# Kernel tuning notes

Measured on AMD Instinct MI355X. Metric: run time of the kernel, lower is better.

Reference implementation:

```python
import jax, jax.numpy as jnp
import numpy as np

LEVEL = 256
BLOCKS = 8
THRESH = 10.0


def setup_inputs() -> dict:
    key = jax.random.key(0)
    img = jax.random.randint(key, (16, 1024, 1024), 0, LEVEL).astype(jnp.float32)
    return {"img": img}


def _clahe(img):
    B, H, W = img.shape
    bm, bn = H // BLOCKS, W // BLOCKS
    v = img.astype(jnp.int32)  # pixel values 0..255, used as histogram bins

    # ---- per-block histograms via one flat scatter-add (segment_sum) ----
    bi = jnp.arange(H) // bm                      # block row per pixel row
    bj = jnp.arange(W) // bn                      # block col per pixel col
    blk = bi[:, None] * BLOCKS + bj[None, :]      # [H, W] block id
    seg = (jnp.arange(B)[:, None, None] * (BLOCKS * BLOCKS) + blk[None]) * LEVEL + v
    hists = jax.ops.segment_sum(
        jnp.ones((B * H * W,), jnp.float32), seg.reshape(-1),
        num_segments=B * BLOCKS * BLOCKS * LEVEL)
    hists = hists.reshape(B, BLOCKS, BLOCKS, LEVEL)

    # ---- clip histogram: redistribute excess above threshold uniformly ----
    # threshold_value = sum(hists)/LEVEL*threshold ; block sum is bm*bn exactly
    tv = (bm * bn) / LEVEL * THRESH
    total_extra = jnp.sum(jnp.maximum(hists - tv, 0.0), axis=-1, keepdims=True)
    mean_extra = total_extra / LEVEL
    # int() truncation of non-negative values == floor
    clip = jnp.floor(jnp.where(hists >= tv, tv + mean_extra, hists + mean_extra))

    # ---- CDF -> uint8 mapping table per block ----
    cdf = jnp.cumsum(clip, axis=-1) * ((LEVEL - 1) / (bm * bn))
    maps = (jnp.floor(cdf).astype(jnp.int32) % 256).astype(jnp.float32)  # [B,BLOCKS,BLOCKS,LEVEL]

    # ---- per-pixel bilinear blend of 2x2 neighboring block maps ----
    ii = jnp.arange(H, dtype=jnp.float32)
    jj = jnp.arange(W, dtype=jnp.float32)
    # Python int() truncates toward zero, so r,c are always >= 0
    r = jnp.trunc((ii - bm / 2) / bm).astype(jnp.int32)   # [H]
    c = jnp.trunc((jj - bn / 2) / bn).astype(jnp.int32)   # [W]
    x1 = (ii - (r.astype(jnp.float32) + 0.5) * bm) / bm   # [H]
    y1 = (jj - (c.astype(jnp.float32) + 0.5) * bn) / bn   # [W]
    rp = jnp.minimum(r + 1, BLOCKS - 1)
    cp = jnp.minimum(c + 1, BLOCKS - 1)
    # on last block row/col the original falls back to 1-D / nearest interp:
    x1e = jnp.where(r >= BLOCKS - 1, 0.0, x1)[:, None]    # [H,1]
    y1e = jnp.where(c >= BLOCKS - 1, 0.0, y1)[None, :]    # [1,W]

    bidx = jnp.arange(B)[:, None, None]

    def gather(rr, cc):  # maps[b, rr[i], cc[j], v[b,i,j]] -> [B,H,W]
        return maps[bidx, rr[None, :, None], cc[None, None, :], v]

    lu = gather(r, c)
    lb = gather(rp, c)
    ru = gather(r, cp)
    rb = gather(rp, cp)
    out = (1 - y1e) * ((1 - x1e) * lu + x1e * lb) + y1e * ((1 - x1e) * ru + x1e * rb)
    # final .astype('uint8') cast
    return (jnp.trunc(out).astype(jnp.int32) % 256).astype(jnp.float32)


def reference(img) -> jnp.ndarray:
    return _clahe(img)
```

## Files before the change

### kernel.cpp

```cpp
#include <hip/hip_runtime.h>
#include <hip/hip_bf16.h>

#define LEVEL 256
#define BLOCKS 8

__global__ __launch_bounds__(256) void clahe_hist_kernel(const float* __restrict__ img,
                                                         float* __restrict__ maps) {
    __shared__ int   hist[256];
    __shared__ float red[256];
    __shared__ float scan[256];
    __shared__ float s_me;

    const int t   = threadIdx.x;
    const int bid = blockIdx.x;
    const int b   = bid >> 6;
    const int blk = bid & 63;
    const int br  = blk >> 3;
    const int bc  = blk & 7;

    hist[t] = 0;
    __syncthreads();

    const size_t base = (size_t)b * 1048576 + (size_t)(br * 128) * 1024 + (size_t)(bc * 128);
    const float* p = img + base;
    for (int it = 0; it < 16; ++it) {
        int idx = it * 256 + t;
        int y   = idx >> 5;
        int x   = (idx & 31) * 4;
        float4 v = *(const float4*)(p + (size_t)y * 1024 + x);
        atomicAdd(&hist[(int)v.x], 1);
        atomicAdd(&hist[(int)v.y], 1);
        atomicAdd(&hist[(int)v.z], 1);
        atomicAdd(&hist[(int)v.w], 1);
    }
    __syncthreads();

    const float tv = 640.0f;
    float h = (float)hist[t];
    float extra = fmaxf(h - tv, 0.0f);
    red[t] = extra;
    __syncthreads();
    for (int off = 128; off > 0; off >>= 1) {
        if (t < off) red[t] += red[t + off];
        __syncthreads();
    }
    if (t == 0) s_me = red[0] * (1.0f / 256.0f);
    __syncthreads();
    const float me = s_me;
    float clip = floorf(((h >= tv) ? tv : h) + me);

    scan[t] = clip;
    __syncthreads();
    for (int off = 1; off < 256; off <<= 1) {
        float add = (t >= off) ? scan[t - off] : 0.0f;
        __syncthreads();
        scan[t] += add;
        __syncthreads();
    }
    float cdf = scan[t] * (255.0f / 16384.0f);
    int m = ((int)floorf(cdf)) & 255;
    maps[(size_t)bid * 256 + t] = (float)m;
}

__global__ __launch_bounds__(256) void clahe_map_kernel(const float* __restrict__ img,
                                                        const float* __restrict__ maps,
                                                        float* __restrict__ out) {
#pragma clang fp contract(off)
    __shared__ float m_lu[256], m_lb[256], m_ru[256], m_rb[256];

    const int t  = threadIdx.x;
    const int b  = blockIdx.z;
    const int i0 = blockIdx.y * 64;
    const int j0 = blockIdx.x * 64;

    const int r  = (i0 >= 64) ? ((i0 - 64) >> 7) : 0;
    const int c  = (j0 >= 64) ? ((j0 - 64) >> 7) : 0;
    const int rp = min(r + 1, BLOCKS - 1);
    const int cp = min(c + 1, BLOCKS - 1);
    const bool rEdge = (r >= BLOCKS - 1);
    const bool cEdge = (c >= BLOCKS - 1);

    const float* mb = maps + (size_t)b * 64 * 256;
    m_lu[t] = mb[(r  * 8 + c ) * 256 + t];
    m_lb[t] = mb[(rp * 8 + c ) * 256 + t];
    m_ru[t] = mb[(r  * 8 + cp) * 256 + t];
    m_rb[t] = mb[(rp * 8 + cp) * 256 + t];
    __syncthreads();

    const size_t ibase = (size_t)b * 1048576;
    const int row_in = t >> 4;
    const int col4   = (t & 15) * 4;

    for (int it = 0; it < 4; ++it) {
        const int i = i0 + it * 16 + row_in;
        const int j = j0 + col4;
        const float4 px = *(const float4*)(img + ibase + (size_t)i * 1024 + j);

        float x1 = rEdge ? 0.0f : ((float)i - (float)(r * 128 + 64)) * 0.0078125f;

        float vals[4] = {px.x, px.y, px.z, px.w};
        float4 o4;
        float* ov = (float*)&o4;
        for (int k = 0; k < 4; ++k) {
            const int jj = j + k;
            float y1 = cEdge ? 0.0f : ((float)jj - (float)(c * 128 + 64)) * 0.0078125f;
            const int vv = (int)vals[k];
            const float lu = m_lu[vv];
            const float lb = m_lb[vv];
            const float ru = m_ru[vv];
            const float rb = m_rb[vv];
            float o = (1.0f - y1) * ((1.0f - x1) * lu + x1 * lb)
                    + y1 * ((1.0f - x1) * ru + x1 * rb);
            ov[k] = (float)(((int)o) & 255);
        }
        *(float4*)(out + ibase + (size_t)i * 1024 + j) = o4;
    }
}

extern "C" void kernel_launch(void* const* d_in, const int* in_sizes, int n_in,
                              void* d_out, int out_size, void* d_ws, size_t ws_size,
                              hipStream_t stream) {
    const float* img = (const float*)d_in[0];
    float* out = (float*)d_out;
    float* maps = (float*)d_ws;

    clahe_hist_kernel<<<dim3(1024), dim3(256), 0, stream>>>(img, maps);
    clahe_map_kernel<<<dim3(16, 16, 16), dim3(256), 0, stream>>>(img, maps, out);
}
```

Baseline: 125.4 us.

## Cache uint8 copy of image in hist pass and pack four maps into float4 LDS

While building histograms, the first kernel also writes a uint8 copy of the image into workspace. The map kernel then reads that compact copy instead of the float image, cutting its input traffic to a quarter. It also interleaves the four neighbouring block maps into one float4 shared-memory table, so each pixel needs a single LDS load. The cost is an extra 16 MB written in the hist kernel, and the fast path runs only if the workspace is large enough.

```diff
diff --git a/kernel.cpp b/kernel.cpp
--- a/kernel.cpp
+++ b/kernel.cpp
@@ -5,7 +5,8 @@
 #define BLOCKS 8
 
 __global__ __launch_bounds__(256) void clahe_hist_kernel(const float* __restrict__ img,
-                                                         float* __restrict__ maps) {
+                                                         float* __restrict__ maps,
+                                                         unsigned char* __restrict__ u8img) {
     __shared__ int   hist[256];
     __shared__ float red[256];
     __shared__ float scan[256];
@@ -23,15 +24,23 @@
 
     const size_t base = (size_t)b * 1048576 + (size_t)(br * 128) * 1024 + (size_t)(bc * 128);
     const float* p = img + base;
+    unsigned char* q8 = u8img ? (u8img + base) : nullptr;
     for (int it = 0; it < 16; ++it) {
         int idx = it * 256 + t;
         int y   = idx >> 5;
         int x   = (idx & 31) * 4;
         float4 v = *(const float4*)(p + (size_t)y * 1024 + x);
-        atomicAdd(&hist[(int)v.x], 1);
-        atomicAdd(&hist[(int)v.y], 1);
-        atomicAdd(&hist[(int)v.z], 1);
-        atomicAdd(&hist[(int)v.w], 1);
+        int va = (int)v.x, vb = (int)v.y, vc = (int)v.z, vd = (int)v.w;
+        atomicAdd(&hist[va], 1);
+        atomicAdd(&hist[vb], 1);
+        atomicAdd(&hist[vc], 1);
+        atomicAdd(&hist[vd], 1);
+        if (q8) {
+            uchar4 pk;
+            pk.x = (unsigned char)va; pk.y = (unsigned char)vb;
+            pk.z = (unsigned char)vc; pk.w = (unsigned char)vd;
+            *(uchar4*)(q8 + (size_t)y * 1024 + x) = pk;
+        }
     }
     __syncthreads();
 
@@ -62,11 +71,13 @@
     maps[(size_t)bid * 256 + t] = (float)m;
 }
 
-__global__ __launch_bounds__(256) void clahe_map_kernel(const float* __restrict__ img,
+template <bool U8>
+__global__ __launch_bounds__(256) void clahe_map_kernel(const float* __restrict__ imgf,
+                                                        const unsigned char* __restrict__ img8,
                                                         const float* __restrict__ maps,
                                                         float* __restrict__ out) {
 #pragma clang fp contract(off)
-    __shared__ float m_lu[256], m_lb[256], m_ru[256], m_rb[256];
+    __shared__ float4 m4[256];
 
     const int t  = threadIdx.x;
     const int b  = blockIdx.z;
@@ -81,10 +92,13 @@
     const bool cEdge = (c >= BLOCKS - 1);
 
     const float* mb = maps + (size_t)b * 64 * 256;
-    m_lu[t] = mb[(r  * 8 + c ) * 256 + t];
-    m_lb[t] = mb[(rp * 8 + c ) * 256 + t];
-    m_ru[t] = mb[(r  * 8 + cp) * 256 + t];
-    m_rb[t] = mb[(rp * 8 + cp) * 256 + t];
+    {
+        float lu = mb[(r  * 8 + c ) * 256 + t];
+        float lb = mb[(rp * 8 + c ) * 256 + t];
+        float ru = mb[(r  * 8 + cp) * 256 + t];
+        float rb = mb[(rp * 8 + cp) * 256 + t];
+        m4[t] = make_float4(lu, lb, ru, rb);
+    }
     __syncthreads();
 
     const size_t ibase = (size_t)b * 1048576;
@@ -94,23 +108,27 @@
     for (int it = 0; it < 4; ++it) {
         const int i = i0 + it * 16 + row_in;
         const int j = j0 + col4;
-        const float4 px = *(const float4*)(img + ibase + (size_t)i * 1024 + j);
 
-        float x1 = rEdge ? 0.0f : ((float)i - (float)(r * 128 + 64)) * 0.0078125f;
+        int vv[4];
+        if (U8) {
+            uchar4 px = *(const uchar4*)(img8 + ibase + (size_t)i * 1024 + j);
+            vv[0] = px.x; vv[1] = px.y; vv[2] = px.z; vv[3] = px.w;
+        } else {
+            float4 px = *(const float4*)(imgf + ibase + (size_t)i * 1024 + j);
+            vv[0] = (int)px.x; vv[1] = (int)px.y; vv[2] = (int)px.z; vv[3] = (int)px.w;
+        }
 
-        float vals[4] = {px.x, px.y, px.z, px.w};
+        const float x1  = rEdge ? 0.0f : ((float)i - (float)(r * 128 + 64)) * 0.0078125f;
+        const float x0  = 1.0f - x1;
+
         float4 o4;
         float* ov = (float*)&o4;
         for (int k = 0; k < 4; ++k) {
             const int jj = j + k;
-            float y1 = cEdge ? 0.0f : ((float)jj - (float)(c * 128 + 64)) * 0.0078125f;
-            const int vv = (int)vals[k];
-            const float lu = m_lu[vv];
-            const float lb = m_lb[vv];
-            const float ru = m_ru[vv];
-            const float rb = m_rb[vv];
-            float o = (1.0f - y1) * ((1.0f - x1) * lu + x1 * lb)
-                    + y1 * ((1.0f - x1) * ru + x1 * rb);
+            const float y1 = cEdge ? 0.0f : ((float)jj - (float)(c * 128 + 64)) * 0.0078125f;
+            const float4 q = m4[vv[k]];
+            float o = (1.0f - y1) * (x0 * q.x + x1 * q.y)
+                    + y1 * (x0 * q.z + x1 * q.w);
             ov[k] = (float)(((int)o) & 255);
         }
         *(float4*)(out + ibase + (size_t)i * 1024 + j) = o4;
@@ -124,6 +142,17 @@
     float* out = (float*)d_out;
     float* maps = (float*)d_ws;
 
-    clahe_hist_kernel<<<dim3(1024), dim3(256), 0, stream>>>(img, maps);
-    clahe_map_kernel<<<dim3(16, 16, 16), dim3(256), 0, stream>>>(img, maps, out);
+    const size_t maps_bytes = (size_t)1024 * 256 * sizeof(float);
+    const size_t u8_bytes   = (size_t)16 * 1024 * 1024;
+    const bool use_u8 = ws_size >= maps_bytes + u8_bytes;
+    unsigned char* u8img = use_u8 ? ((unsigned char*)d_ws + maps_bytes) : nullptr;
+
+    clahe_hist_kernel<<<dim3(1024), dim3(256), 0, stream>>>(img, maps, u8img);
+    if (use_u8) {
+        clahe_map_kernel<true><<<dim3(16, 16, 16), dim3(256), 0, stream>>>(
+            nullptr, u8img, maps, out);
+    } else {
+        clahe_map_kernel<false><<<dim3(16, 16, 16), dim3(256), 0, stream>>>(
+            img, nullptr, maps, out);
+    }
 }
```

Result: no change. 124.0 us (-1.1%).

## Stage image as uint8 in workspace, per-wave histograms, packed LUT table

Applied to the files above, without the earlier changes.

The histogram kernel now writes a uint8 copy of the image to workspace, so the map kernel reads 1 byte per pixel instead of 4. The histogram is split into four per-wave copies to reduce shared-atomic contention. The map kernel packs the four neighbouring LUT entries into one 32-bit word so each pixel needs a single LDS read. Non-temporal loads and stores are added for the streaming accesses. The trade-off is an extra 16 MB write in the first kernel, and the workspace must be large enough to hold the byte image.

```diff
diff --git a/kernel.cpp b/kernel.cpp
--- a/kernel.cpp
+++ b/kernel.cpp
@@ -5,40 +5,55 @@
 #define BLOCKS 8
 
 __global__ __launch_bounds__(256) void clahe_hist_kernel(const float* __restrict__ img,
-                                                         float* __restrict__ maps) {
-    __shared__ int   hist[256];
+                                                         float* __restrict__ maps,
+                                                         unsigned char* __restrict__ u8img) {
+    __shared__ int   hist[4][256];
     __shared__ float red[256];
     __shared__ float scan[256];
     __shared__ float s_me;
 
-    const int t   = threadIdx.x;
-    const int bid = blockIdx.x;
-    const int b   = bid >> 6;
-    const int blk = bid & 63;
-    const int br  = blk >> 3;
-    const int bc  = blk & 7;
+    const int t    = threadIdx.x;
+    const int wave = t >> 6;
+    const int bid  = blockIdx.x;
+    const int b    = bid >> 6;
+    const int blk  = bid & 63;
+    const int br   = blk >> 3;
+    const int bc   = blk & 7;
 
-    hist[t] = 0;
+    hist[0][t] = 0; hist[1][t] = 0; hist[2][t] = 0; hist[3][t] = 0;
     __syncthreads();
 
     const size_t base = (size_t)b * 1048576 + (size_t)(br * 128) * 1024 + (size_t)(bc * 128);
     const float* p = img + base;
+    unsigned char* q8 = u8img + base;
+    int* myhist = hist[wave];
+#pragma unroll
     for (int it = 0; it < 16; ++it) {
         int idx = it * 256 + t;
         int y   = idx >> 5;
         int x   = (idx & 31) * 4;
-        float4 v = *(const float4*)(p + (size_t)y * 1024 + x);
-        atomicAdd(&hist[(int)v.x], 1);
-        atomicAdd(&hist[(int)v.y], 1);
-        atomicAdd(&hist[(int)v.z], 1);
-        atomicAdd(&hist[(int)v.w], 1);
+        const float* src = p + (size_t)y * 1024 + x;
+        float4 v;
+        v.x = __builtin_nontemporal_load(src + 0);
+        v.y = __builtin_nontemporal_load(src + 1);
+        v.z = __builtin_nontemporal_load(src + 2);
+        v.w = __builtin_nontemporal_load(src + 3);
+        int va = (int)v.x, vb = (int)v.y, vc = (int)v.z, vd = (int)v.w;
+        atomicAdd(&myhist[va], 1);
+        atomicAdd(&myhist[vb], 1);
+        atomicAdd(&myhist[vc], 1);
+        atomicAdd(&myhist[vd], 1);
+        uchar4 pk;
+        pk.x = (unsigned char)va; pk.y = (unsigned char)vb;
+        pk.z = (unsigned char)vc; pk.w = (unsigned char)vd;
+        *(uchar4*)(q8 + (size_t)y * 1024 + x) = pk;
     }
     __syncthreads();
 
+    float h = (float)(hist[0][t] + hist[1][t] + hist[2][t] + hist[3][t]);
+
     const float tv = 640.0f;
-    float h = (float)hist[t];
-    float extra = fmaxf(h - tv, 0.0f);
-    red[t] = extra;
+    red[t] = fmaxf(h - tv, 0.0f);
     __syncthreads();
     for (int off = 128; off > 0; off >>= 1) {
         if (t < off) red[t] += red[t + off];
@@ -58,15 +73,14 @@
         __syncthreads();
     }
     float cdf = scan[t] * (255.0f / 16384.0f);
-    int m = ((int)floorf(cdf)) & 255;
-    maps[(size_t)bid * 256 + t] = (float)m;
+    maps[(size_t)bid * 256 + t] = (float)(((int)floorf(cdf)) & 255);
 }
 
-__global__ __launch_bounds__(256) void clahe_map_kernel(const float* __restrict__ img,
+__global__ __launch_bounds__(256) void clahe_map_kernel(const unsigned char* __restrict__ img8,
                                                         const float* __restrict__ maps,
                                                         float* __restrict__ out) {
 #pragma clang fp contract(off)
-    __shared__ float m_lu[256], m_lb[256], m_ru[256], m_rb[256];
+    __shared__ unsigned int tbl[256];
 
     const int t  = threadIdx.x;
     const int b  = blockIdx.z;
@@ -81,39 +95,50 @@
     const bool cEdge = (c >= BLOCKS - 1);
 
     const float* mb = maps + (size_t)b * 64 * 256;
-    m_lu[t] = mb[(r  * 8 + c ) * 256 + t];
-    m_lb[t] = mb[(rp * 8 + c ) * 256 + t];
-    m_ru[t] = mb[(r  * 8 + cp) * 256 + t];
-    m_rb[t] = mb[(rp * 8 + cp) * 256 + t];
+    {
+        unsigned lu = (unsigned)(int)mb[(r  * 8 + c ) * 256 + t];
+        unsigned lb = (unsigned)(int)mb[(rp * 8 + c ) * 256 + t];
+        unsigned ru = (unsigned)(int)mb[(r  * 8 + cp) * 256 + t];
+        unsigned rb = (unsigned)(int)mb[(rp * 8 + cp) * 256 + t];
+        tbl[t] = lu | (lb << 8) | (ru << 16) | (rb << 24);
+    }
     __syncthreads();
 
     const size_t ibase = (size_t)b * 1048576;
     const int row_in = t >> 4;
     const int col4   = (t & 15) * 4;
 
+#pragma unroll
     for (int it = 0; it < 4; ++it) {
         const int i = i0 + it * 16 + row_in;
         const int j = j0 + col4;
-        const float4 px = *(const float4*)(img + ibase + (size_t)i * 1024 + j);
 
-        float x1 = rEdge ? 0.0f : ((float)i - (float)(r * 128 + 64)) * 0.0078125f;
+        uchar4 px = *(const uchar4*)(img8 + ibase + (size_t)i * 1024 + j);
+        int vv[4] = { px.x, px.y, px.z, px.w };
 
-        float vals[4] = {px.x, px.y, px.z, px.w};
+        const float x1 = rEdge ? 0.0f : ((float)i - (float)(r * 128 + 64)) * 0.0078125f;
+        const float x0 = 1.0f - x1;
+
         float4 o4;
         float* ov = (float*)&o4;
+#pragma unroll
         for (int k = 0; k < 4; ++k) {
             const int jj = j + k;
-            float y1 = cEdge ? 0.0f : ((float)jj - (float)(c * 128 + 64)) * 0.0078125f;
-            const int vv = (int)vals[k];
-            const float lu = m_lu[vv];
-            const float lb = m_lb[vv];
-            const float ru = m_ru[vv];
-            const float rb = m_rb[vv];
-            float o = (1.0f - y1) * ((1.0f - x1) * lu + x1 * lb)
-                    + y1 * ((1.0f - x1) * ru + x1 * rb);
+            const float y1 = cEdge ? 0.0f : ((float)jj - (float)(c * 128 + 64)) * 0.0078125f;
+            unsigned mv = tbl[vv[k]];
+            float lu = (float)(mv & 255u);
+            float lb = (float)((mv >> 8) & 255u);
+            float ru = (float)((mv >> 16) & 255u);
+            float rb = (float)(mv >> 24);
+            float o = (1.0f - y1) * (x0 * lu + x1 * lb)
+                    + y1 * (x0 * ru + x1 * rb);
             ov[k] = (float)(((int)o) & 255);
         }
-        *(float4*)(out + ibase + (size_t)i * 1024 + j) = o4;
+        float* dst = out + ibase + (size_t)i * 1024 + j;
+        __builtin_nontemporal_store(o4.x, dst + 0);
+        __builtin_nontemporal_store(o4.y, dst + 1);
+        __builtin_nontemporal_store(o4.z, dst + 2);
+        __builtin_nontemporal_store(o4.w, dst + 3);
     }
 }
 
@@ -121,9 +146,10 @@
                               void* d_out, int out_size, void* d_ws, size_t ws_size,
                               hipStream_t stream) {
     const float* img = (const float*)d_in[0];
-    float* out = (float*)d_out;
+    float* out  = (float*)d_out;
     float* maps = (float*)d_ws;
+    unsigned char* u8img = (unsigned char*)d_ws + (size_t)1024 * 256 * sizeof(float);
 
-    clahe_hist_kernel<<<dim3(1024), dim3(256), 0, stream>>>(img, maps);
-    clahe_map_kernel<<<dim3(16, 16, 16), dim3(256), 0, stream>>>(img, maps, out);
+    clahe_hist_kernel<<<dim3(1024), dim3(256), 0, stream>>>(img, maps, u8img);
+    clahe_map_kernel<<<dim3(16, 16, 16), dim3(256), 0, stream>>>(u8img, maps, out);
 }
```

Measured after the change: 125.3 us. Within noise of the previous version (-0.1%).
